# Kernel optimization log

Measured on AMD Instinct MI355X. Metric: run time of the kernel, lower is better.

## Reference

```python
import jax, jax.numpy as jnp
import numpy as np

IN_F, OUT_F, EMBED = 128, 64, 32
ALPHA = 0.2  # LeakyReLU negative slope


def setup_inputs() -> dict:
    key = jax.random.key(0)
    ks = jax.random.split(key, 8)
    N = 8192
    inp = {
        "input": jax.random.normal(ks[0], (N, IN_F), dtype=jnp.float32),
        "adj": jax.random.uniform(ks[1], (N, N), dtype=jnp.float32),
        "intent_embeds": jax.random.normal(ks[2], (N, EMBED), dtype=jnp.float32),
        # learned parameters
        "W": jax.random.normal(ks[3], (IN_F, OUT_F), dtype=jnp.float32) * 0.1,
        "a": jax.random.normal(ks[4], (2 * OUT_F, 1), dtype=jnp.float32) * 0.1,
        "intent_w": jax.random.normal(ks[5], (1, 2 * EMBED), dtype=jnp.float32) * 0.1,
        "intent_b": jnp.zeros((1,), dtype=jnp.float32),
        "intent_beta": jnp.asarray(0.1, dtype=jnp.float32),
    }
    return inp


def reference(input, adj, intent_embeds, W, a, intent_w, intent_b, intent_beta):
    # h = X W  -> (N, out)
    h = input @ W
    # spatial score e[i,j] = leakyrelu(a1 . h_i + a2 . h_j)  (decomposed, no NxNx2F tensor)
    a1, a2 = a[:OUT_F, 0], a[OUT_F:, 0]
    e_src = h @ a1  # (N,)
    e_dst = h @ a2  # (N,)
    spatial_e = jax.nn.leaky_relu(e_src[:, None] + e_dst[None, :], negative_slope=ALPHA)
    # intent score: Linear([intent_i; intent_j]) = wi.intent_i + wj.intent_j + b
    wi, wj = intent_w[0, :EMBED], intent_w[0, EMBED:]
    ii = intent_embeds @ wi  # (N,)
    jj = intent_embeds @ wj  # (N,)
    intent_e = ii[:, None] + jj[None, :] + intent_b[0]
    total_e = spatial_e + intent_beta * intent_e
    # NOTE: original code computes zero_vec but never masks with adj -> unmasked softmax
    attention = jax.nn.softmax(total_e, axis=0)  # softmax over dim 0, as in source
    h_prime = attention @ h  # (N, out)
    return jax.nn.elu(h_prime)  # concat=True path
```

## Files before the change

kernel.cpp:

```cpp
#include <hip/hip_runtime.h>
#include <hip/hip_bf16.h>

#define NN 8192
#define INF 128
#define OUTF 64
#define EMB 32
#define LOG2E 1.4426950408889634f
#define ISPLIT 64
#define ICH (NN / ISPLIT)
#define MGUARD 64.0f

typedef __attribute__((ext_vector_type(8))) short bf16x8;
typedef __attribute__((ext_vector_type(4))) float f32x4;

#define OFF_HB   0u
#define OFF_UW   1048576u
#define OFF_E12  1114112u
#define OFF_SP   1179648u
#define OFF_PQ   3276800u
#define OFF_PART 3342336u


__global__ __launch_bounds__(256) void k1_h(
    const float* __restrict__ input, const float* __restrict__ Wm,
    const float* __restrict__ av, const float* __restrict__ embeds,
    const float* __restrict__ intw, const float* __restrict__ betap,
    ushort* __restrict__ hB, float2* __restrict__ UW,
    float2* __restrict__ e12)
{
    __shared__ float hl[16][65];
    const int t    = threadIdx.x;
    const int wid  = t >> 6;
    const int lane = t & 63;
    const int blk  = blockIdx.x;
    const int i0 = blk * 16 + wid * 4;

    const float a1 = av[lane];
    const float a2 = av[64 + lane];
    const float* x0 = input + (size_t)i0 * INF;

    float acc0 = 0.f, acc1 = 0.f, acc2 = 0.f, acc3 = 0.f;
#pragma unroll 4
    for (int k = 0; k < INF; k += 4) {
        const float wk0 = Wm[(k + 0) * OUTF + lane];
        const float wk1 = Wm[(k + 1) * OUTF + lane];
        const float wk2 = Wm[(k + 2) * OUTF + lane];
        const float wk3 = Wm[(k + 3) * OUTF + lane];
        const float4 xa = *(const float4*)(x0 + k);
        const float4 xb = *(const float4*)(x0 + INF + k);
        const float4 xc = *(const float4*)(x0 + 2 * INF + k);
        const float4 xd = *(const float4*)(x0 + 3 * INF + k);
        acc0 = fmaf(xa.x, wk0, acc0); acc0 = fmaf(xa.y, wk1, acc0);
        acc0 = fmaf(xa.z, wk2, acc0); acc0 = fmaf(xa.w, wk3, acc0);
        acc1 = fmaf(xb.x, wk0, acc1); acc1 = fmaf(xb.y, wk1, acc1);
        acc1 = fmaf(xb.z, wk2, acc1); acc1 = fmaf(xb.w, wk3, acc1);
        acc2 = fmaf(xc.x, wk0, acc2); acc2 = fmaf(xc.y, wk1, acc2);
        acc2 = fmaf(xc.z, wk2, acc2); acc2 = fmaf(xc.w, wk3, acc2);
        acc3 = fmaf(xd.x, wk0, acc3); acc3 = fmaf(xd.y, wk1, acc3);
        acc3 = fmaf(xd.z, wk2, acc3); acc3 = fmaf(xd.w, wk3, acc3);
    }

    hl[wid * 4 + 0][lane] = acc0;
    hl[wid * 4 + 1][lane] = acc1;
    hl[wid * 4 + 2][lane] = acc2;
    hl[wid * 4 + 3][lane] = acc3;

    float accs[4] = {acc0, acc1, acc2, acc3};
#pragma unroll
    for (int r = 0; r < 4; ++r) {
        float v1 = accs[r] * a1;
        float v2 = accs[r] * a2;
#pragma unroll
        for (int o = 32; o > 0; o >>= 1) {
            v1 += __shfl_xor(v1, o);
            v2 += __shfl_xor(v2, o);
        }
        float p = 0.f;
        if (lane < EMB) p = embeds[(size_t)(i0 + r) * EMB + lane] * intw[lane];
#pragma unroll
        for (int o = 16; o > 0; o >>= 1) p += __shfl_xor(p, o);

        if (lane == 0) {
            const float q = betap[0] * p;
            UW[i0 + r] = make_float2(
                __builtin_amdgcn_exp2f((v1 + q) * LOG2E),
                __builtin_amdgcn_exp2f((0.2f * v1 + q) * LOG2E));
            e12[i0 + r] = make_float2(v2 * LOG2E, 0.2f * v2 * LOG2E);
        }
    }

    __syncthreads();
    if (t < 128) {
        const int rr = t >> 6;
        const int of = t & 63;
        const int nb = of >> 4;
        const int r2 = of & 15;
        const int tile = blk >> 1;
        const int g = (blk & 1) * 2 + rr;
        const int l = g * 16 + r2;
        union { bf16x8 v; ushort us[8]; } pk;
#pragma unroll
        for (int e = 0; e < 8; ++e) {
            __hip_bfloat16 b = __float2bfloat16(hl[rr * 8 + e][of]);
            pk.us[e] = *(ushort*)&b;
        }
        *(bf16x8*)(hB + (size_t)(((nb * 256 + tile) * 64 + l) * 8)) = pk.v;
    }
}

__global__ __launch_bounds__(256) void k2_colsum(
    const float2* __restrict__ UW, const float2* __restrict__ e12,
    float* __restrict__ Spart)
{
    const int j0 = blockIdx.x * 256 + threadIdx.x;
    const int j1 = j0 + 4096;
    const float2 ea = e12[j0];
    const float2 eb = e12[j1];
    const float Ma = fmaxf(ea.x, ea.y) + MGUARD;
    const float Mb = fmaxf(eb.x, eb.y) + MGUARD;
    const float Pa = __builtin_amdgcn_exp2f(ea.x - Ma);
    const float Qa = __builtin_amdgcn_exp2f(ea.y - Ma);
    const float Pb = __builtin_amdgcn_exp2f(eb.x - Mb);
    const float Qb = __builtin_amdgcn_exp2f(eb.y - Mb);

    const float* up = (const float*)UW + (size_t)blockIdx.y * ICH * 2;
    float sa = 0.f, sb = 0.f;
#pragma unroll 8
    for (int rr = 0; rr < ICH * 2; rr += 4) {
        const float4 c = *(const float4*)(up + rr);
        sa += fmaxf(c.x * Pa, c.y * Qa);
        sa += fmaxf(c.z * Pa, c.w * Qa);
        sb += fmaxf(c.x * Pb, c.y * Qb);
        sb += fmaxf(c.z * Pb, c.w * Qb);
    }
    Spart[(size_t)blockIdx.y * NN + j0] = sa;
    Spart[(size_t)blockIdx.y * NN + j1] = sb;
}

__global__ __launch_bounds__(256) void k3_cc(
    const float2* __restrict__ e12, const float* __restrict__ Spart,
    float2* __restrict__ PQn)
{
    const int j = blockIdx.x * 256 + threadIdx.x;
    float s = 0.f;
#pragma unroll
    for (int k = 0; k < ISPLIT; ++k) s += Spart[(size_t)k * NN + j];
    const float2 e = e12[j];
    const float Mj = fmaxf(e.x, e.y) + MGUARD;
    const float cc = Mj + __builtin_amdgcn_logf(s);
    PQn[j] = make_float2(__builtin_amdgcn_exp2f(e.x - cc),
                         __builtin_amdgcn_exp2f(e.y - cc));
}

__global__ __launch_bounds__(256) void k4_mm(
    const float2* __restrict__ UW, const float2* __restrict__ PQn,
    const ushort* __restrict__ hB, float* __restrict__ part, int jch)
{
    const int wid  = threadIdx.x >> 6;
    const int lane = threadIdx.x & 63;
    const int r = lane & 15;
    const int g = lane >> 4;
    const int ibase = blockIdx.x * 128 + wid * 32;

    const float2 c0 = UW[ibase + r];
    const float2 c1 = UW[ibase + 16 + r];

    const int jb = blockIdx.y * jch;
    const int je = jb + jch;

    f32x4 a00 = {0,0,0,0}, a01 = {0,0,0,0}, a02 = {0,0,0,0}, a03 = {0,0,0,0};
    f32x4 a10 = {0,0,0,0}, a11 = {0,0,0,0}, a12 = {0,0,0,0}, a13 = {0,0,0,0};

    for (int j0 = jb; j0 < je; j0 += 32) {
        const int jj = j0 + g * 8;
        const float* pqp = (const float*)(PQn + jj);
        const float4 q0 = *(const float4*)(pqp);
        const float4 q1 = *(const float4*)(pqp + 4);
        const float4 q2 = *(const float4*)(pqp + 8);
        const float4 q3 = *(const float4*)(pqp + 12);

        float e00 = fmaxf(c0.x * q0.x, c0.y * q0.y);
        float e01 = fmaxf(c0.x * q0.z, c0.y * q0.w);
        float e02 = fmaxf(c0.x * q1.x, c0.y * q1.y);
        float e03 = fmaxf(c0.x * q1.z, c0.y * q1.w);
        float e04 = fmaxf(c0.x * q2.x, c0.y * q2.y);
        float e05 = fmaxf(c0.x * q2.z, c0.y * q2.w);
        float e06 = fmaxf(c0.x * q3.x, c0.y * q3.y);
        float e07 = fmaxf(c0.x * q3.z, c0.y * q3.w);

        float e10 = fmaxf(c1.x * q0.x, c1.y * q0.y);
        float e11 = fmaxf(c1.x * q0.z, c1.y * q0.w);
        float e12v= fmaxf(c1.x * q1.x, c1.y * q1.y);
        float e13 = fmaxf(c1.x * q1.z, c1.y * q1.w);
        float e14 = fmaxf(c1.x * q2.x, c1.y * q2.y);
        float e15 = fmaxf(c1.x * q2.z, c1.y * q2.w);
        float e16 = fmaxf(c1.x * q3.x, c1.y * q3.y);
        float e17 = fmaxf(c1.x * q3.z, c1.y * q3.w);

        union { bf16x8 v; unsigned u[4]; } A0, A1;
        asm("v_cvt_pk_bf16_f32 %0, %1, %2" : "=v"(A0.u[0]) : "v"(e00), "v"(e01));
        asm("v_cvt_pk_bf16_f32 %0, %1, %2" : "=v"(A0.u[1]) : "v"(e02), "v"(e03));
        asm("v_cvt_pk_bf16_f32 %0, %1, %2" : "=v"(A0.u[2]) : "v"(e04), "v"(e05));
        asm("v_cvt_pk_bf16_f32 %0, %1, %2" : "=v"(A0.u[3]) : "v"(e06), "v"(e07));
        asm("v_cvt_pk_bf16_f32 %0, %1, %2" : "=v"(A1.u[0]) : "v"(e10), "v"(e11));
        asm("v_cvt_pk_bf16_f32 %0, %1, %2" : "=v"(A1.u[1]) : "v"(e12v),"v"(e13));
        asm("v_cvt_pk_bf16_f32 %0, %1, %2" : "=v"(A1.u[2]) : "v"(e14), "v"(e15));
        asm("v_cvt_pk_bf16_f32 %0, %1, %2" : "=v"(A1.u[3]) : "v"(e16), "v"(e17));

        const int tile = j0 >> 5;
        const ushort* hb = hB + (size_t)(tile * 64 + lane) * 8;
        const bf16x8 b0 = *(const bf16x8*)(hb);
        const bf16x8 b1 = *(const bf16x8*)(hb + 256 * 64 * 8);
        const bf16x8 b2 = *(const bf16x8*)(hb + 2 * 256 * 64 * 8);
        const bf16x8 b3 = *(const bf16x8*)(hb + 3 * 256 * 64 * 8);

        a00 = __builtin_amdgcn_mfma_f32_16x16x32_bf16(A0.v, b0, a00, 0, 0, 0);
        a01 = __builtin_amdgcn_mfma_f32_16x16x32_bf16(A0.v, b1, a01, 0, 0, 0);
        a02 = __builtin_amdgcn_mfma_f32_16x16x32_bf16(A0.v, b2, a02, 0, 0, 0);
        a03 = __builtin_amdgcn_mfma_f32_16x16x32_bf16(A0.v, b3, a03, 0, 0, 0);
        a10 = __builtin_amdgcn_mfma_f32_16x16x32_bf16(A1.v, b0, a10, 0, 0, 0);
        a11 = __builtin_amdgcn_mfma_f32_16x16x32_bf16(A1.v, b1, a11, 0, 0, 0);
        a12 = __builtin_amdgcn_mfma_f32_16x16x32_bf16(A1.v, b2, a12, 0, 0, 0);
        a13 = __builtin_amdgcn_mfma_f32_16x16x32_bf16(A1.v, b3, a13, 0, 0, 0);
    }

    float* pout = part + (size_t)blockIdx.y * (NN * OUTF);
#pragma unroll
    for (int m = 0; m < 4; ++m) {
        const int row0 = ibase + g * 4 + m;
        const int row1 = ibase + 16 + g * 4 + m;
        pout[(size_t)row0 * OUTF + 0  + r] = a00[m];
        pout[(size_t)row0 * OUTF + 16 + r] = a01[m];
        pout[(size_t)row0 * OUTF + 32 + r] = a02[m];
        pout[(size_t)row0 * OUTF + 48 + r] = a03[m];
        pout[(size_t)row1 * OUTF + 0  + r] = a10[m];
        pout[(size_t)row1 * OUTF + 16 + r] = a11[m];
        pout[(size_t)row1 * OUTF + 32 + r] = a12[m];
        pout[(size_t)row1 * OUTF + 48 + r] = a13[m];
    }
}

__global__ __launch_bounds__(256) void k5_combine(
    const float* __restrict__ part, float* __restrict__ out, int JS)
{
    const int base = (blockIdx.x * 256 + threadIdx.x) * 4;
    float4 v = make_float4(0.f, 0.f, 0.f, 0.f);
    for (int s = 0; s < JS; ++s) {
        const float4 p = *(const float4*)(part + (size_t)s * (NN * OUTF) + base);
        v.x += p.x; v.y += p.y; v.z += p.z; v.w += p.w;
    }
    float4 o;
    o.x = v.x > 0.f ? v.x : (__builtin_amdgcn_exp2f(v.x * LOG2E) - 1.f);
    o.y = v.y > 0.f ? v.y : (__builtin_amdgcn_exp2f(v.y * LOG2E) - 1.f);
    o.z = v.z > 0.f ? v.z : (__builtin_amdgcn_exp2f(v.z * LOG2E) - 1.f);
    o.w = v.w > 0.f ? v.w : (__builtin_amdgcn_exp2f(v.w * LOG2E) - 1.f);
    *(float4*)(out + base) = o;
}

extern "C" void kernel_launch(void* const* d_in, const int* in_sizes, int n_in,
                              void* d_out, int out_size, void* d_ws, size_t ws_size,
                              hipStream_t stream)
{
    const float* input  = (const float*)d_in[0];
    const float* embeds = (const float*)d_in[2];
    const float* Wm     = (const float*)d_in[3];
    const float* av     = (const float*)d_in[4];
    const float* intw   = (const float*)d_in[5];
    const float* betap  = (const float*)d_in[7];
    float* out = (float*)d_out;

    char* ws = (char*)d_ws;
    ushort* hB   = (ushort*)(ws + OFF_HB);
    float2* UW   = (float2*)(ws + OFF_UW);
    float2* e12  = (float2*)(ws + OFF_E12);
    float* Spart = (float*)(ws + OFF_SP);
    float2* PQn  = (float2*)(ws + OFF_PQ);
    float* part  = (float*)(ws + OFF_PART);

    int JS = 8;
    while (JS > 1 &&
           (size_t)OFF_PART + (size_t)JS * NN * OUTF * sizeof(float) > ws_size)
        JS >>= 1;
    const int jch = NN / JS;

    k1_h<<<NN / 16, 256, 0, stream>>>(input, Wm, av, embeds, intw, betap,
                                      hB, UW, e12);
    k2_colsum<<<dim3(NN / 512, ISPLIT), 256, 0, stream>>>(UW, e12, Spart);
    k3_cc<<<NN / 256, 256, 0, stream>>>(e12, Spart, PQn);
    k4_mm<<<dim3(NN / 128, JS), 256, 0, stream>>>(UW, PQn, hB, part, jch);
    k5_combine<<<(NN * OUTF) / 1024, 256, 0, stream>>>(part, out, JS);
}
```

Before: 68.04 us.

## Fuse normalization and combine stages using atomics and last-block ELU epilogue

Removes the k3 normalization and k5 combine kernels. Column-sum partials are now accumulated with float atomics into S, which k1 zero-initializes along with the output and the counters. k4 computes normalized P/Q per j-chunk into shared memory, atomically adds its tile into the output, and the last of the 8 j-split blocks per row tile applies ELU. This saves two launches and the partial-buffer traffic, at the cost of atomic contention and non-deterministic summation order.

```diff
diff --git a/kernel.cpp b/kernel.cpp
--- a/kernel.cpp
+++ b/kernel.cpp
@@ -16,9 +16,8 @@
 #define OFF_HB   0u
 #define OFF_UW   1048576u
 #define OFF_E12  1114112u
-#define OFF_SP   1179648u
-#define OFF_PQ   3276800u
-#define OFF_PART 3342336u
+#define OFF_S    1179648u
+#define OFF_CNT  1212416u
 
 
 __global__ __launch_bounds__(256) void k1_h(
@@ -26,7 +25,8 @@
     const float* __restrict__ av, const float* __restrict__ embeds,
     const float* __restrict__ intw, const float* __restrict__ betap,
     ushort* __restrict__ hB, float2* __restrict__ UW,
-    float2* __restrict__ e12)
+    float2* __restrict__ e12, float* __restrict__ S,
+    float* __restrict__ out, int* __restrict__ cnt)
 {
     __shared__ float hl[16][65];
     const int t    = threadIdx.x;
@@ -34,6 +34,13 @@
     const int lane = t & 63;
     const int blk  = blockIdx.x;
     const int i0 = blk * 16 + wid * 4;
+
+    if (t < 16) S[blk * 16 + t] = 0.f;
+    if (blk == 0 && t < 64) cnt[t] = 0;
+    {
+        const float4 z = make_float4(0.f, 0.f, 0.f, 0.f);
+        *(float4*)(out + (size_t)blk * 1024 + t * 4) = z;
+    }
 
     const float a1 = av[lane];
     const float a2 = av[64 + lane];
@@ -110,7 +117,7 @@
 
 __global__ __launch_bounds__(256) void k2_colsum(
     const float2* __restrict__ UW, const float2* __restrict__ e12,
-    float* __restrict__ Spart)
+    float* __restrict__ S)
 {
     const int j0 = blockIdx.x * 256 + threadIdx.x;
     const int j1 = j0 + 4096;
@@ -133,47 +140,44 @@
         sb += fmaxf(c.x * Pb, c.y * Qb);
         sb += fmaxf(c.z * Pb, c.w * Qb);
     }
-    Spart[(size_t)blockIdx.y * NN + j0] = sa;
-    Spart[(size_t)blockIdx.y * NN + j1] = sb;
-}
-
-__global__ __launch_bounds__(256) void k3_cc(
-    const float2* __restrict__ e12, const float* __restrict__ Spart,
-    float2* __restrict__ PQn)
-{
-    const int j = blockIdx.x * 256 + threadIdx.x;
-    float s = 0.f;
-#pragma unroll
-    for (int k = 0; k < ISPLIT; ++k) s += Spart[(size_t)k * NN + j];
-    const float2 e = e12[j];
-    const float Mj = fmaxf(e.x, e.y) + MGUARD;
-    const float cc = Mj + __builtin_amdgcn_logf(s);
-    PQn[j] = make_float2(__builtin_amdgcn_exp2f(e.x - cc),
-                         __builtin_amdgcn_exp2f(e.y - cc));
+    unsafeAtomicAdd(&S[j0], sa);
+    unsafeAtomicAdd(&S[j1], sb);
 }
 
 __global__ __launch_bounds__(256) void k4_mm(
-    const float2* __restrict__ UW, const float2* __restrict__ PQn,
-    const ushort* __restrict__ hB, float* __restrict__ part, int jch)
-{
+    const float2* __restrict__ UW, const float2* __restrict__ e12,
+    const float* __restrict__ S, const ushort* __restrict__ hB,
+    float* __restrict__ out, int* __restrict__ cnt)
+{
+    __shared__ float2 pq[1024];
+    __shared__ int isLast;
+
     const int wid  = threadIdx.x >> 6;
     const int lane = threadIdx.x & 63;
     const int r = lane & 15;
     const int g = lane >> 4;
-    const int ibase = blockIdx.x * 128 + wid * 32;
-
+    const int mt = blockIdx.x;
+    const int jb = blockIdx.y * 1024;
+
+    for (int c = threadIdx.x; c < 1024; c += 256) {
+        const float2 e = e12[jb + c];
+        const float M = fmaxf(e.x, e.y) + MGUARD;
+        const float inv = 1.0f / S[jb + c];
+        pq[c] = make_float2(__builtin_amdgcn_exp2f(e.x - M) * inv,
+                            __builtin_amdgcn_exp2f(e.y - M) * inv);
+    }
+    __syncthreads();
+
+    const int ibase = mt * 128 + wid * 32;
     const float2 c0 = UW[ibase + r];
     const float2 c1 = UW[ibase + 16 + r];
 
-    const int jb = blockIdx.y * jch;
-    const int je = jb + jch;
-
     f32x4 a00 = {0,0,0,0}, a01 = {0,0,0,0}, a02 = {0,0,0,0}, a03 = {0,0,0,0};
     f32x4 a10 = {0,0,0,0}, a11 = {0,0,0,0}, a12 = {0,0,0,0}, a13 = {0,0,0,0};
 
-    for (int j0 = jb; j0 < je; j0 += 32) {
+    for (int j0 = jb; j0 < jb + 1024; j0 += 32) {
         const int jj = j0 + g * 8;
-        const float* pqp = (const float*)(PQn + jj);
+        const float* pqp = (const float*)&pq[jj - jb];
         const float4 q0 = *(const float4*)(pqp);
         const float4 q1 = *(const float4*)(pqp + 4);
         const float4 q2 = *(const float4*)(pqp + 8);
@@ -224,37 +228,36 @@
         a13 = __builtin_amdgcn_mfma_f32_16x16x32_bf16(A1.v, b3, a13, 0, 0, 0);
     }
 
-    float* pout = part + (size_t)blockIdx.y * (NN * OUTF);
 #pragma unroll
     for (int m = 0; m < 4; ++m) {
         const int row0 = ibase + g * 4 + m;
         const int row1 = ibase + 16 + g * 4 + m;
-        pout[(size_t)row0 * OUTF + 0  + r] = a00[m];
-        pout[(size_t)row0 * OUTF + 16 + r] = a01[m];
-        pout[(size_t)row0 * OUTF + 32 + r] = a02[m];
-        pout[(size_t)row0 * OUTF + 48 + r] = a03[m];
-        pout[(size_t)row1 * OUTF + 0  + r] = a10[m];
-        pout[(size_t)row1 * OUTF + 16 + r] = a11[m];
-        pout[(size_t)row1 * OUTF + 32 + r] = a12[m];
-        pout[(size_t)row1 * OUTF + 48 + r] = a13[m];
-    }
-}
-
-__global__ __launch_bounds__(256) void k5_combine(
-    const float* __restrict__ part, float* __restrict__ out, int JS)
-{
-    const int base = (blockIdx.x * 256 + threadIdx.x) * 4;
-    float4 v = make_float4(0.f, 0.f, 0.f, 0.f);
-    for (int s = 0; s < JS; ++s) {
-        const float4 p = *(const float4*)(part + (size_t)s * (NN * OUTF) + base);
-        v.x += p.x; v.y += p.y; v.z += p.z; v.w += p.w;
-    }
-    float4 o;
-    o.x = v.x > 0.f ? v.x : (__builtin_amdgcn_exp2f(v.x * LOG2E) - 1.f);
-    o.y = v.y > 0.f ? v.y : (__builtin_amdgcn_exp2f(v.y * LOG2E) - 1.f);
-    o.z = v.z > 0.f ? v.z : (__builtin_amdgcn_exp2f(v.z * LOG2E) - 1.f);
-    o.w = v.w > 0.f ? v.w : (__builtin_amdgcn_exp2f(v.w * LOG2E) - 1.f);
-    *(float4*)(out + base) = o;
+        unsafeAtomicAdd(&out[(size_t)row0 * OUTF + 0  + r], a00[m]);
+        unsafeAtomicAdd(&out[(size_t)row0 * OUTF + 16 + r], a01[m]);
+        unsafeAtomicAdd(&out[(size_t)row0 * OUTF + 32 + r], a02[m]);
+        unsafeAtomicAdd(&out[(size_t)row0 * OUTF + 48 + r], a03[m]);
+        unsafeAtomicAdd(&out[(size_t)row1 * OUTF + 0  + r], a10[m]);
+        unsafeAtomicAdd(&out[(size_t)row1 * OUTF + 16 + r], a11[m]);
+        unsafeAtomicAdd(&out[(size_t)row1 * OUTF + 32 + r], a12[m]);
+        unsafeAtomicAdd(&out[(size_t)row1 * OUTF + 48 + r], a13[m]);
+    }
+
+    __threadfence();
+    __syncthreads();
+    if (threadIdx.x == 0) {
+        const int old = __hip_atomic_fetch_add(&cnt[mt], 1, __ATOMIC_ACQ_REL,
+                                               __HIP_MEMORY_SCOPE_AGENT);
+        isLast = (old == 7);
+    }
+    __syncthreads();
+    if (isLast) {
+        for (int k = threadIdx.x; k < 128 * OUTF; k += 256) {
+            float* p = &out[(size_t)mt * 128 * OUTF + k];
+            const float v = __hip_atomic_load(p, __ATOMIC_RELAXED,
+                                              __HIP_MEMORY_SCOPE_AGENT);
+            *p = v > 0.f ? v : (__builtin_amdgcn_exp2f(v * LOG2E) - 1.f);
+        }
+    }
 }
 
 extern "C" void kernel_launch(void* const* d_in, const int* in_sizes, int n_in,
@@ -270,23 +273,14 @@
     float* out = (float*)d_out;
 
     char* ws = (char*)d_ws;
-    ushort* hB   = (ushort*)(ws + OFF_HB);
-    float2* UW   = (float2*)(ws + OFF_UW);
-    float2* e12  = (float2*)(ws + OFF_E12);
-    float* Spart = (float*)(ws + OFF_SP);
-    float2* PQn  = (float2*)(ws + OFF_PQ);
-    float* part  = (float*)(ws + OFF_PART);
-
-    int JS = 8;
-    while (JS > 1 &&
-           (size_t)OFF_PART + (size_t)JS * NN * OUTF * sizeof(float) > ws_size)
-        JS >>= 1;
-    const int jch = NN / JS;
+    ushort* hB  = (ushort*)(ws + OFF_HB);
+    float2* UW  = (float2*)(ws + OFF_UW);
+    float2* e12 = (float2*)(ws + OFF_E12);
+    float* S    = (float*)(ws + OFF_S);
+    int*   cnt  = (int*)(ws + OFF_CNT);
 
     k1_h<<<NN / 16, 256, 0, stream>>>(input, Wm, av, embeds, intw, betap,
-                                      hB, UW, e12);
-    k2_colsum<<<dim3(NN / 512, ISPLIT), 256, 0, stream>>>(UW, e12, Spart);
-    k3_cc<<<NN / 256, 256, 0, stream>>>(e12, Spart, PQn);
-    k4_mm<<<dim3(NN / 128, JS), 256, 0, stream>>>(UW, PQn, hB, part, jch);
-    k5_combine<<<(NN * OUTF) / 1024, 256, 0, stream>>>(part, out, JS);
-}
+                                      hB, UW, e12, S, out, cnt);
+    k2_colsum<<<dim3(NN / 512, ISPLIT), 256, 0, stream>>>(UW, e12, S);
+    k4_mm<<<dim3(64, 8), 256, 0, stream>>>(UW, e12, S, hB, out, cnt);
+}
```

Result: slower. 97.69 us (+43.6%).

## Replace partial column-sum buffer and k3 kernel with atomics and LDS-fused normalization

Applied to the files above, without the earlier changes.

The column-sum kernel now accumulates its partial sums directly into a zeroed S vector with float atomics, replacing the per-split partial buffer. The separate normalization kernel that produced PQn is removed. Instead, each k4 block computes its own chunk of normalized P/Q coefficients into shared memory before the matmul loop. This saves one launch and the 2 MB partial write/read, at the cost of atomic contention, recomputation of exp per k4 block, and a JS floor of 4 so the LDS array (2048 float2) can hold a chunk.

```diff
diff --git a/kernel.cpp b/kernel.cpp
--- a/kernel.cpp
+++ b/kernel.cpp
@@ -16,9 +16,8 @@
 #define OFF_HB   0u
 #define OFF_UW   1048576u
 #define OFF_E12  1114112u
-#define OFF_SP   1179648u
-#define OFF_PQ   3276800u
-#define OFF_PART 3342336u
+#define OFF_S    1179648u
+#define OFF_PART 1212416u
 
 
 __global__ __launch_bounds__(256) void k1_h(
@@ -26,7 +25,7 @@
     const float* __restrict__ av, const float* __restrict__ embeds,
     const float* __restrict__ intw, const float* __restrict__ betap,
     ushort* __restrict__ hB, float2* __restrict__ UW,
-    float2* __restrict__ e12)
+    float2* __restrict__ e12, float* __restrict__ S)
 {
     __shared__ float hl[16][65];
     const int t    = threadIdx.x;
@@ -34,6 +33,8 @@
     const int lane = t & 63;
     const int blk  = blockIdx.x;
     const int i0 = blk * 16 + wid * 4;
+
+    if (t < 16) S[blk * 16 + t] = 0.f;
 
     const float a1 = av[lane];
     const float a2 = av[64 + lane];
@@ -110,7 +111,7 @@
 
 __global__ __launch_bounds__(256) void k2_colsum(
     const float2* __restrict__ UW, const float2* __restrict__ e12,
-    float* __restrict__ Spart)
+    float* __restrict__ S)
 {
     const int j0 = blockIdx.x * 256 + threadIdx.x;
     const int j1 = j0 + 4096;
@@ -133,47 +134,42 @@
         sb += fmaxf(c.x * Pb, c.y * Qb);
         sb += fmaxf(c.z * Pb, c.w * Qb);
     }
-    Spart[(size_t)blockIdx.y * NN + j0] = sa;
-    Spart[(size_t)blockIdx.y * NN + j1] = sb;
-}
-
-__global__ __launch_bounds__(256) void k3_cc(
-    const float2* __restrict__ e12, const float* __restrict__ Spart,
-    float2* __restrict__ PQn)
-{
-    const int j = blockIdx.x * 256 + threadIdx.x;
-    float s = 0.f;
-#pragma unroll
-    for (int k = 0; k < ISPLIT; ++k) s += Spart[(size_t)k * NN + j];
-    const float2 e = e12[j];
-    const float Mj = fmaxf(e.x, e.y) + MGUARD;
-    const float cc = Mj + __builtin_amdgcn_logf(s);
-    PQn[j] = make_float2(__builtin_amdgcn_exp2f(e.x - cc),
-                         __builtin_amdgcn_exp2f(e.y - cc));
+    unsafeAtomicAdd(&S[j0], sa);
+    unsafeAtomicAdd(&S[j1], sb);
 }
 
 __global__ __launch_bounds__(256) void k4_mm(
-    const float2* __restrict__ UW, const float2* __restrict__ PQn,
-    const ushort* __restrict__ hB, float* __restrict__ part, int jch)
-{
+    const float2* __restrict__ UW, const float2* __restrict__ e12,
+    const float* __restrict__ S, const ushort* __restrict__ hB,
+    float* __restrict__ part, int jch)
+{
+    __shared__ float2 pq[2048];
+
     const int wid  = threadIdx.x >> 6;
     const int lane = threadIdx.x & 63;
     const int r = lane & 15;
     const int g = lane >> 4;
     const int ibase = blockIdx.x * 128 + wid * 32;
+    const int jb = blockIdx.y * jch;
+
+    for (int c = threadIdx.x; c < jch; c += 256) {
+        const float2 e = e12[jb + c];
+        const float M = fmaxf(e.x, e.y) + MGUARD;
+        const float inv = 1.0f / S[jb + c];
+        pq[c] = make_float2(__builtin_amdgcn_exp2f(e.x - M) * inv,
+                            __builtin_amdgcn_exp2f(e.y - M) * inv);
+    }
+    __syncthreads();
 
     const float2 c0 = UW[ibase + r];
     const float2 c1 = UW[ibase + 16 + r];
 
-    const int jb = blockIdx.y * jch;
-    const int je = jb + jch;
-
     f32x4 a00 = {0,0,0,0}, a01 = {0,0,0,0}, a02 = {0,0,0,0}, a03 = {0,0,0,0};
     f32x4 a10 = {0,0,0,0}, a11 = {0,0,0,0}, a12 = {0,0,0,0}, a13 = {0,0,0,0};
 
-    for (int j0 = jb; j0 < je; j0 += 32) {
+    for (int j0 = jb; j0 < jb + jch; j0 += 32) {
         const int jj = j0 + g * 8;
-        const float* pqp = (const float*)(PQn + jj);
+        const float* pqp = (const float*)&pq[jj - jb];
         const float4 q0 = *(const float4*)(pqp);
         const float4 q1 = *(const float4*)(pqp + 4);
         const float4 q2 = *(const float4*)(pqp + 8);
@@ -270,23 +266,21 @@
     float* out = (float*)d_out;
 
     char* ws = (char*)d_ws;
-    ushort* hB   = (ushort*)(ws + OFF_HB);
-    float2* UW   = (float2*)(ws + OFF_UW);
-    float2* e12  = (float2*)(ws + OFF_E12);
-    float* Spart = (float*)(ws + OFF_SP);
-    float2* PQn  = (float2*)(ws + OFF_PQ);
-    float* part  = (float*)(ws + OFF_PART);
+    ushort* hB  = (ushort*)(ws + OFF_HB);
+    float2* UW  = (float2*)(ws + OFF_UW);
+    float2* e12 = (float2*)(ws + OFF_E12);
+    float* S    = (float*)(ws + OFF_S);
+    float* part = (float*)(ws + OFF_PART);
 
     int JS = 8;
-    while (JS > 1 &&
+    while (JS > 4 &&
            (size_t)OFF_PART + (size_t)JS * NN * OUTF * sizeof(float) > ws_size)
         JS >>= 1;
     const int jch = NN / JS;
 
     k1_h<<<NN / 16, 256, 0, stream>>>(input, Wm, av, embeds, intw, betap,
-                                      hB, UW, e12);
-    k2_colsum<<<dim3(NN / 512, ISPLIT), 256, 0, stream>>>(UW, e12, Spart);
-    k3_cc<<<NN / 256, 256, 0, stream>>>(e12, Spart, PQn);
-    k4_mm<<<dim3(NN / 128, JS), 256, 0, stream>>>(UW, PQn, hB, part, jch);
+                                      hB, UW, e12, S);
+    k2_colsum<<<dim3(NN / 512, ISPLIT), 256, 0, stream>>>(UW, e12, S);
+    k4_mm<<<dim3(NN / 128, JS), 256, 0, stream>>>(UW, e12, S, hB, part, jch);
     k5_combine<<<(NN * OUTF) / 1024, 256, 0, stream>>>(part, out, JS);
 }
```

Result: faster. 56.95 us (median of 2 runs) (-16.3%).
